# Performance work log

Measured on AMD Instinct MI355X. Metric: run time of the kernel, lower is better.

## Reference

```python
import jax, jax.numpy as jnp
import numpy as np

B, Z, A, D = 2048, 128, 4, 50000
EPS = 1e-8


def setup_inputs() -> dict:
    key = jax.random.key(0)
    k1, k2, k3, k4, k5 = jax.random.split(key, 5)
    return {
        "batch_x": jax.random.normal(k1, (B, Z), dtype=jnp.float32),
        "batch_next": jax.random.normal(k2, (B, Z), dtype=jnp.float32),
        "keys": jax.random.normal(k3, (A, D, Z), dtype=jnp.float32),
        "vals": jax.random.normal(k4, (A, D, Z), dtype=jnp.float32),
        "batch_a": jax.random.randint(k5, (B,), 0, A, dtype=jnp.int64),
    }


def _dnd_lookup(q, keys_a, vals_a):
    # q: [B, Z] (L2-normalized), keys_a: [D, Z], vals_a: [D, Z]
    kn = keys_a / (jnp.linalg.norm(keys_a, axis=-1, keepdims=True) + EPS)
    sims = jnp.einsum("bz,dz->bd", q, kn)          # cosine similarity [B, D]
    w = jax.nn.softmax(sims, axis=-1)                # attention over dictionary
    return jnp.einsum("bd,dz->bz", w, vals_a)       # [B, Z]


def reference(batch_x, batch_next, keys, vals, batch_a):
    # Per-sample routed DND lookup: each sample queries the memory of its action,
    # then MSE loss vs batch_next (eval-mode trainBatch; memory write is a state
    # mutation done after the loss and does not affect the returned value).
    qn = batch_x / (jnp.linalg.norm(batch_x, axis=-1, keepdims=True) + EPS)
    a_space = keys.shape[0]
    pred = jnp.zeros_like(batch_x)
    for a in range(a_space):  # small fixed loop over distinct memories
        pred_a = _dnd_lookup(qn, keys[a], vals[a])
        pred = jnp.where((batch_a == a)[:, None], pred_a, pred)
    return jnp.mean((pred - batch_next) ** 2)
```

## Files before the change

kernel.cpp:

```cpp
#include <hip/hip_runtime.h>
#include <stdint.h>

#define B_N 2048
#define Z_N 128
#define A_N 4
#define D_N 50000
#define EPS_F 1e-8f

typedef __attribute__((ext_vector_type(8))) short short8;
typedef __attribute__((ext_vector_type(4))) short bf4;
typedef __attribute__((ext_vector_type(4))) float f32x4;

__device__ __forceinline__ unsigned short f2bf(float f) {
  unsigned int u = __builtin_bit_cast(unsigned int, f);
  u += 0x7FFFu + ((u >> 16) & 1u);
  return (unsigned short)(u >> 16);
}

__global__ void k_norm(const float* __restrict__ keys, const float* __restrict__ x,
                       const int* __restrict__ act,
                       unsigned short* __restrict__ kn, unsigned short* __restrict__ qnb,
                       int* __restrict__ counts, int* __restrict__ lists) {
  int w = threadIdx.x >> 6, lane = threadIdx.x & 63;
  size_t row = (size_t)blockIdx.x * 4 + w;
  bool isq = row >= (size_t)A_N * D_N;
  size_t r = isq ? row - (size_t)A_N * D_N : row;
  const float* src = (isq ? x : keys) + r * Z_N;
  const float2 v = ((const float2*)src)[lane];
  float ss = v.x * v.x + v.y * v.y;
#pragma unroll
  for (int m = 1; m < 64; m <<= 1) ss += __shfl_xor(ss, m);
  float inv = 1.0f / (sqrtf(ss) + EPS_F);
  unsigned int packed = ((unsigned int)f2bf(v.y * inv) << 16) | f2bf(v.x * inv);
  unsigned short* dst = (isq ? qnb : kn) + r * Z_N;
  ((unsigned int*)dst)[lane] = packed;
  if (isq && lane == 0) {
    int a = act[r];
    int pos = atomicAdd(&counts[a], 1);
    lists[a * B_N + pos] = (int)r;
  }
}

__global__ void k_vtrans(const float* __restrict__ vals, unsigned short* __restrict__ vt) {
  __shared__ float tile[64][65];
  int a = blockIdx.z, d0 = blockIdx.x * 64, z0 = blockIdx.y * 64;
  int t = threadIdx.x;
  int r = t >> 4, c4 = (t & 15) * 4;
#pragma unroll
  for (int i = 0; i < 4; ++i) {
    int dr = r + i * 16, d = d0 + dr;
    if (d < D_N) {
      const float4 v = *(const float4*)(vals + ((size_t)a * D_N + d) * Z_N + z0 + c4);
      tile[dr][c4 + 0] = v.x; tile[dr][c4 + 1] = v.y;
      tile[dr][c4 + 2] = v.z; tile[dr][c4 + 3] = v.w;
    }
  }
  __syncthreads();
  int zz = t >> 2, dg = (t & 3) * 16;
  if (d0 + dg < D_N) {
    union { unsigned short u[16]; uint4 q[2]; } pk;
#pragma unroll
    for (int j = 0; j < 16; ++j) pk.u[j] = f2bf(tile[dg + j][zz]);
    unsigned short* dst = vt + ((size_t)a * Z_N + z0 + zz) * D_N + d0 + dg;
    ((uint4*)dst)[0] = pk.q[0];
    ((uint4*)dst)[1] = pk.q[1];
  }
}

#define TILE_B 128
#define KT 32
#define CHUNK 800
#define NITER 25
#define NCHUNK 63
#define KL_S 140
#define VL_S 36

__global__ void k_worklist(const int* __restrict__ counts, int* __restrict__ work) {
  int t0 = (counts[0] + TILE_B - 1) / TILE_B;
  int t1 = (counts[1] + TILE_B - 1) / TILE_B;
  int t2 = (counts[2] + TILE_B - 1) / TILE_B;
  int t3 = (counts[3] + TILE_B - 1) / TILE_B;
  int T = t0 + t1 + t2 + t3;
  int total = T * NCHUNK;
  if (threadIdx.x == 0) work[0] = total;
  for (int i = threadIdx.x; i < total; i += 256) {
    int c = i / T, j = i - c * T;
    int a, ty;
    if (j < t0)                { a = 0; ty = j; }
    else if (j < t0 + t1)      { a = 1; ty = j - t0; }
    else if (j < t0 + t1 + t2) { a = 2; ty = j - t0 - t1; }
    else                       { a = 3; ty = j - t0 - t1 - t2; }
    work[1 + i] = a | (ty << 2) | (c << 8);
  }
}

__launch_bounds__(256, 2)
__global__ void k_flash(const unsigned short* __restrict__ kn,
                        const unsigned short* __restrict__ vt,
                        const unsigned short* __restrict__ qnb,
                        const int* __restrict__ counts,
                        const int* __restrict__ lists,
                        const int* __restrict__ work,
                        float* __restrict__ acc,
                        float* __restrict__ sume) {
  int total = work[0];
  if ((int)blockIdx.x >= total) return;
  int wi = work[1 + blockIdx.x];
  int a = wi & 3, ty = (wi >> 2) & 63, chunk = wi >> 8;
  int nb = counts[a];

  __shared__ unsigned short Kl[KT * KL_S];
  __shared__ unsigned short Vl[128 * VL_S];

  int t = threadIdx.x;
  int w = t >> 6, lane = t & 63;
  int lq = lane >> 4, ln = lane & 15;

  const unsigned short* kn_a = kn + (size_t)a * D_N * Z_N;
  const unsigned short* vt_a = vt + (size_t)a * Z_N * D_N;
  const int* list_a = lists + a * B_N;

  short8 qf[2][4];
#pragma unroll
  for (int mt = 0; mt < 2; ++mt) {
    int g = ty * TILE_B + w * 32 + mt * 16 + ln;
    bool valid = g < nb;
    int si = valid ? list_a[g] : 0;
#pragma unroll
    for (int c = 0; c < 4; ++c) {
      short8 s = (short8){0,0,0,0,0,0,0,0};
      if (valid) s = *(const short8*)(qnb + (size_t)si * Z_N + c * 32 + lq * 8);
      qf[mt][c] = s;
    }
  }

  f32x4 O[2][8];
#pragma unroll
  for (int mt = 0; mt < 2; ++mt)
#pragma unroll
    for (int zt = 0; zt < 8; ++zt) O[mt][zt] = (f32x4){0.f, 0.f, 0.f, 0.f};
  float rs[2] = {0.f, 0.f};

  int d_base = chunk * CHUNK;
  int sk_key = t >> 3, sk_z = (t & 7) * 16;
  int sv_z = t >> 1, sv_k = (t & 1) * 16;

  const uint4 z4 = {0u, 0u, 0u, 0u};
  uint4 kA, kB, vA, vB;

  {
    int key = d_base + sk_key;
    bool kok = key < D_N;
    const uint4* ksrc = (const uint4*)(kn_a + (size_t)key * Z_N + sk_z);
    kA = kok ? ksrc[0] : z4;
    kB = kok ? ksrc[1] : z4;
    int kk = d_base + sv_k;
    const unsigned short* vsrc = vt_a + (size_t)sv_z * D_N + kk;
    vA = (kk < D_N)     ? *(const uint4*)vsrc       : z4;
    vB = (kk + 8 < D_N) ? *(const uint4*)(vsrc + 8) : z4;
  }

  for (int kt = 0; kt < NITER; ++kt) {
    int d0 = d_base + kt * KT;
    __syncthreads();
    {
      uint4* kd = (uint4*)&Kl[sk_key * KL_S + sk_z];
      kd[0] = kA; kd[1] = kB;
      uint4* vd = (uint4*)&Vl[sv_z * VL_S + sv_k];
      vd[0] = vA; vd[1] = vB;
    }
    __syncthreads();
    if (kt + 1 < NITER) {
      int d1 = d0 + KT;
      int key = d1 + sk_key;
      bool kok = key < D_N;
      const uint4* ksrc = (const uint4*)(kn_a + (size_t)key * Z_N + sk_z);
      kA = kok ? ksrc[0] : z4;
      kB = kok ? ksrc[1] : z4;
      int kk = d1 + sv_k;
      const unsigned short* vsrc = vt_a + (size_t)sv_z * D_N + kk;
      vA = (kk < D_N)     ? *(const uint4*)vsrc       : z4;
      vB = (kk + 8 < D_N) ? *(const uint4*)(vsrc + 8) : z4;
    }

    f32x4 ST[2][2];
#pragma unroll
    for (int nt = 0; nt < 2; ++nt) {
      short8 kf[4];
#pragma unroll
      for (int c = 0; c < 4; ++c)
        kf[c] = *(const short8*)&Kl[(nt * 16 + ln) * KL_S + c * 32 + lq * 8];
#pragma unroll
      for (int mt = 0; mt < 2; ++mt) {
        f32x4 s4 = (f32x4){0.f, 0.f, 0.f, 0.f};
#pragma unroll
        for (int c = 0; c < 4; ++c)
          s4 = __builtin_amdgcn_mfma_f32_16x16x32_bf16(kf[c], qf[mt][c], s4, 0, 0, 0);
        ST[nt][mt] = s4;
      }
    }

    bf4 pf[2][2];
#pragma unroll
    for (int nt = 0; nt < 2; ++nt) {
      int kbase = d0 + nt * 16 + lq * 4;
#pragma unroll
      for (int mt = 0; mt < 2; ++mt) {
        float e0 = (kbase + 0) < D_N ? __expf(ST[nt][mt][0]) : 0.f;
        float e1 = (kbase + 1) < D_N ? __expf(ST[nt][mt][1]) : 0.f;
        float e2 = (kbase + 2) < D_N ? __expf(ST[nt][mt][2]) : 0.f;
        float e3 = (kbase + 3) < D_N ? __expf(ST[nt][mt][3]) : 0.f;
        rs[mt] += e0 + e1 + e2 + e3;
        unsigned long long p =
            (unsigned long long)f2bf(e0) |
            ((unsigned long long)f2bf(e1) << 16) |
            ((unsigned long long)f2bf(e2) << 32) |
            ((unsigned long long)f2bf(e3) << 48);
        pf[mt][nt] = __builtin_bit_cast(bf4, p);
      }
    }

#pragma unroll
    for (int zt = 0; zt < 8; ++zt) {
#pragma unroll
      for (int nt = 0; nt < 2; ++nt) {
        bf4 vf = *(const bf4*)&Vl[(zt * 16 + ln) * VL_S + nt * 16 + lq * 4];
        asm volatile("s_nop 1\n\tv_mfma_f32_16x16x16_bf16 %0, %1, %2, %0"
                     : "+v"(O[0][zt]) : "v"(pf[0][nt]), "v"(vf));
        asm volatile("s_nop 1\n\tv_mfma_f32_16x16x16_bf16 %0, %1, %2, %0"
                     : "+v"(O[1][zt]) : "v"(pf[1][nt]), "v"(vf));
      }
    }
  }

#pragma unroll
  for (int mt = 0; mt < 2; ++mt) {
    float v = rs[mt];
    v += __shfl_xor(v, 16);
    v += __shfl_xor(v, 32);
    rs[mt] = v;
  }

#pragma unroll
  for (int mt = 0; mt < 2; ++mt) {
    if (lq == 0) {
      int g = ty * TILE_B + w * 32 + mt * 16 + ln;
      if (g < nb) atomicAdd(&sume[list_a[g]], rs[mt]);
    }
#pragma unroll
    for (int r = 0; r < 4; ++r) {
      int g = ty * TILE_B + w * 32 + mt * 16 + lq * 4 + r;
      if (g < nb) {
        int si = list_a[g];
        float* arow = acc + (size_t)si * Z_N + ln;
#pragma unroll
        for (int zt = 0; zt < 8; ++zt) atomicAdd(arow + zt * 16, O[mt][zt][r]);
      }
    }
  }
}

__global__ void k_loss(const float* __restrict__ acc, const float* __restrict__ sume,
                       const float* __restrict__ nxt, float* __restrict__ loss) {
  __shared__ float ls[4];
  int w = threadIdx.x >> 6, lane = threadIdx.x & 63;
  int row = blockIdx.x * 4 + w;
  float inv = 1.0f / sume[row];
  const float2 p2 = ((const float2*)(acc + (size_t)row * Z_N))[lane];
  const float2 n2 = ((const float2*)(nxt + (size_t)row * Z_N))[lane];
  float dx = p2.x * inv - n2.x, dy = p2.y * inv - n2.y;
  float s = dx * dx + dy * dy;
#pragma unroll
  for (int m = 1; m < 64; m <<= 1) s += __shfl_xor(s, m);
  if (lane == 0) ls[w] = s;
  __syncthreads();
  if (threadIdx.x == 0) atomicAdd(loss, ls[0] + ls[1] + ls[2] + ls[3]);
}

__global__ void k_final(const float* __restrict__ loss, float* __restrict__ out) {
  out[0] = loss[0] * (1.0f / (float)(B_N * Z_N));
}

extern "C" void kernel_launch(void* const* d_in, const int* in_sizes, int n_in,
                              void* d_out, int out_size, void* d_ws, size_t ws_size,
                              hipStream_t stream) {
  const float* x    = (const float*)d_in[0];
  const float* nxt  = (const float*)d_in[1];
  const float* keys = (const float*)d_in[2];
  const float* vals = (const float*)d_in[3];
  const int*   act  = (const int*)d_in[4];

  char* ws = (char*)d_ws;
  unsigned short* qnb = (unsigned short*)(ws + 0);
  float* acc    = (float*)(ws + 1048576);
  float* sume   = (float*)(ws + 2097152);
  int*   counts = (int*)(ws + 2105344);
  float* loss   = (float*)(ws + 2105360);
  int*   lists  = (int*)(ws + 2105376);
  int*   work   = (int*)(ws + 2138144);
  unsigned short* kn = (unsigned short*)(ws + 2146560);
  unsigned short* vt = (unsigned short*)(ws + 53346560);

  hipMemsetAsync(ws + 1048576, 0, 1056800, stream);

  k_norm<<<50512, 256, 0, stream>>>(keys, x, act, kn, qnb, counts, lists);
  k_vtrans<<<dim3(782, 2, A_N), 256, 0, stream>>>(vals, vt);
  k_worklist<<<1, 256, 0, stream>>>(counts, work);
  k_flash<<<1280, 256, 0, stream>>>(kn, vt, qnb, counts, lists, work, acc, sume);
  k_loss<<<512, 256, 0, stream>>>(acc, sume, nxt, loss);
  k_final<<<1, 1, 0, stream>>>(loss, (float*)d_out);
}
```

Before: 452.8 us.

## Restructure flash kernel to 512-thread blocks with double-buffered LDS and fewer splits

The flash-style lookup kernel now uses 512 threads per block, each wave owning 16 query rows instead of 32. Keys and transposed values are staged through double-buffered shared memory, so each iteration needs one barrier instead of two. The key dimension is split into 32 spans of 1568 rather than 63 chunks of 800, which roughly halves the number of partial-result atomics. Routing of samples by action moves out of the normalization kernel into a single-block kernel that counts in shared memory, removing global atomics on the counts. The trade-offs are less register reuse of each LDS fragment per wave and fewer blocks available to fill the GPU.

```diff
diff --git a/kernel.cpp b/kernel.cpp
--- a/kernel.cpp
+++ b/kernel.cpp
@@ -7,6 +7,14 @@
 #define D_N 50000
 #define EPS_F 1e-8f
 
+#define TILE_B 128
+#define KT 32
+#define NSPLIT 32
+#define SPAN 1568
+#define NITER 49
+#define KL_S 140
+#define VL_S 36
+
 typedef __attribute__((ext_vector_type(8))) short short8;
 typedef __attribute__((ext_vector_type(4))) short bf4;
 typedef __attribute__((ext_vector_type(4))) float f32x4;
@@ -18,9 +26,7 @@
 }
 
 __global__ void k_norm(const float* __restrict__ keys, const float* __restrict__ x,
-                       const int* __restrict__ act,
-                       unsigned short* __restrict__ kn, unsigned short* __restrict__ qnb,
-                       int* __restrict__ counts, int* __restrict__ lists) {
+                       unsigned short* __restrict__ kn, unsigned short* __restrict__ qnb) {
   int w = threadIdx.x >> 6, lane = threadIdx.x & 63;
   size_t row = (size_t)blockIdx.x * 4 + w;
   bool isq = row >= (size_t)A_N * D_N;
@@ -34,11 +40,6 @@
   unsigned int packed = ((unsigned int)f2bf(v.y * inv) << 16) | f2bf(v.x * inv);
   unsigned short* dst = (isq ? qnb : kn) + r * Z_N;
   ((unsigned int*)dst)[lane] = packed;
-  if (isq && lane == 0) {
-    int a = act[r];
-    int pos = atomicAdd(&counts[a], 1);
-    lists[a * B_N + pos] = (int)r;
-  }
 }
 
 __global__ void k_vtrans(const float* __restrict__ vals, unsigned short* __restrict__ vt) {
@@ -67,23 +68,25 @@
   }
 }
 
-#define TILE_B 128
-#define KT 32
-#define CHUNK 800
-#define NITER 25
-#define NCHUNK 63
-#define KL_S 140
-#define VL_S 36
-
-__global__ void k_worklist(const int* __restrict__ counts, int* __restrict__ work) {
-  int t0 = (counts[0] + TILE_B - 1) / TILE_B;
-  int t1 = (counts[1] + TILE_B - 1) / TILE_B;
-  int t2 = (counts[2] + TILE_B - 1) / TILE_B;
-  int t3 = (counts[3] + TILE_B - 1) / TILE_B;
+__global__ void k_route(const int* __restrict__ act, int* __restrict__ counts,
+                        int* __restrict__ lists, int* __restrict__ work) {
+  __shared__ int lc[4];
+  int t = threadIdx.x;
+  if (t < 4) lc[t] = 0;
+  __syncthreads();
+  for (int i = t; i < B_N; i += 1024) {
+    int a = act[i];
+    int pos = atomicAdd(&lc[a], 1);
+    lists[a * B_N + pos] = i;
+  }
+  __syncthreads();
+  if (t < 4) counts[t] = lc[t];
+  int t0 = (lc[0] + TILE_B - 1) >> 7, t1 = (lc[1] + TILE_B - 1) >> 7;
+  int t2 = (lc[2] + TILE_B - 1) >> 7, t3 = (lc[3] + TILE_B - 1) >> 7;
   int T = t0 + t1 + t2 + t3;
-  int total = T * NCHUNK;
-  if (threadIdx.x == 0) work[0] = total;
-  for (int i = threadIdx.x; i < total; i += 256) {
+  int total = T * NSPLIT;
+  if (t == 0) work[0] = total;
+  for (int i = t; i < total; i += 1024) {
     int c = i / T, j = i - c * T;
     int a, ty;
     if (j < t0)                { a = 0; ty = j; }
@@ -94,7 +97,7 @@
   }
 }
 
-__launch_bounds__(256, 2)
+__launch_bounds__(512)
 __global__ void k_flash(const unsigned short* __restrict__ kn,
                         const unsigned short* __restrict__ vt,
                         const unsigned short* __restrict__ qnb,
@@ -106,11 +109,11 @@
   int total = work[0];
   if ((int)blockIdx.x >= total) return;
   int wi = work[1 + blockIdx.x];
-  int a = wi & 3, ty = (wi >> 2) & 63, chunk = wi >> 8;
+  int a = wi & 3, ty = (wi >> 2) & 63, span = wi >> 8;
   int nb = counts[a];
 
-  __shared__ unsigned short Kl[KT * KL_S];
-  __shared__ unsigned short Vl[128 * VL_S];
+  __shared__ unsigned short Kl[2][KT * KL_S];
+  __shared__ unsigned short Vl[2][128 * VL_S];
 
   int t = threadIdx.x;
   int w = t >> 6, lane = t & 63;
@@ -120,142 +123,112 @@
   const unsigned short* vt_a = vt + (size_t)a * Z_N * D_N;
   const int* list_a = lists + a * B_N;
 
-  short8 qf[2][4];
-#pragma unroll
-  for (int mt = 0; mt < 2; ++mt) {
-    int g = ty * TILE_B + w * 32 + mt * 16 + ln;
-    bool valid = g < nb;
-    int si = valid ? list_a[g] : 0;
-#pragma unroll
-    for (int c = 0; c < 4; ++c) {
-      short8 s = (short8){0,0,0,0,0,0,0,0};
-      if (valid) s = *(const short8*)(qnb + (size_t)si * Z_N + c * 32 + lq * 8);
-      qf[mt][c] = s;
-    }
-  }
-
-  f32x4 O[2][8];
-#pragma unroll
-  for (int mt = 0; mt < 2; ++mt)
-#pragma unroll
-    for (int zt = 0; zt < 8; ++zt) O[mt][zt] = (f32x4){0.f, 0.f, 0.f, 0.f};
-  float rs[2] = {0.f, 0.f};
-
-  int d_base = chunk * CHUNK;
-  int sk_key = t >> 3, sk_z = (t & 7) * 16;
-  int sv_z = t >> 1, sv_k = (t & 1) * 16;
+  int g0 = ty * TILE_B + w * 16 + ln;
+  bool qvalid = g0 < nb;
+  int si0 = qvalid ? list_a[g0] : 0;
+  short8 qf[4];
+#pragma unroll
+  for (int c = 0; c < 4; ++c) {
+    short8 s = (short8){0,0,0,0,0,0,0,0};
+    if (qvalid) s = *(const short8*)(qnb + (size_t)si0 * Z_N + c * 32 + lq * 8);
+    qf[c] = s;
+  }
+
+  f32x4 O[8];
+#pragma unroll
+  for (int zt = 0; zt < 8; ++zt) O[zt] = (f32x4){0.f, 0.f, 0.f, 0.f};
+  float rs = 0.f;
+
+  int d_base = span * SPAN;
+  int sk_key = t >> 4, sk_z = (t & 15) * 8;
+  int sv_z = t >> 2, sv_k = (t & 3) * 8;
 
   const uint4 z4 = {0u, 0u, 0u, 0u};
-  uint4 kA, kB, vA, vB;
-
-  {
-    int key = d_base + sk_key;
-    bool kok = key < D_N;
-    const uint4* ksrc = (const uint4*)(kn_a + (size_t)key * Z_N + sk_z);
-    kA = kok ? ksrc[0] : z4;
-    kB = kok ? ksrc[1] : z4;
-    int kk = d_base + sv_k;
-    const unsigned short* vsrc = vt_a + (size_t)sv_z * D_N + kk;
-    vA = (kk < D_N)     ? *(const uint4*)vsrc       : z4;
-    vB = (kk + 8 < D_N) ? *(const uint4*)(vsrc + 8) : z4;
-  }
-
+  uint4 kp, vp;
+
+#define LOAD_TILE(d)                                                          \
+  {                                                                           \
+    int key = (d) + sk_key;                                                   \
+    kp = (key < D_N) ? *(const uint4*)(kn_a + (size_t)key * Z_N + sk_z) : z4; \
+    int kk = (d) + sv_k;                                                      \
+    vp = (kk < D_N) ? *(const uint4*)(vt_a + (size_t)sv_z * D_N + kk) : z4;   \
+  }
+#define STORE_TILE(p)                                                         \
+  {                                                                           \
+    *(uint4*)&Kl[p][sk_key * KL_S + sk_z] = kp;                               \
+    *(uint4*)&Vl[p][sv_z * VL_S + sv_k] = vp;                                 \
+  }
+
+  LOAD_TILE(d_base);
+  STORE_TILE(0);
+  LOAD_TILE(d_base + KT);
+  __syncthreads();
+
+  int p = 0;
   for (int kt = 0; kt < NITER; ++kt) {
     int d0 = d_base + kt * KT;
-    __syncthreads();
-    {
-      uint4* kd = (uint4*)&Kl[sk_key * KL_S + sk_z];
-      kd[0] = kA; kd[1] = kB;
-      uint4* vd = (uint4*)&Vl[sv_z * VL_S + sv_k];
-      vd[0] = vA; vd[1] = vB;
-    }
-    __syncthreads();
     if (kt + 1 < NITER) {
-      int d1 = d0 + KT;
-      int key = d1 + sk_key;
-      bool kok = key < D_N;
-      const uint4* ksrc = (const uint4*)(kn_a + (size_t)key * Z_N + sk_z);
-      kA = kok ? ksrc[0] : z4;
-      kB = kok ? ksrc[1] : z4;
-      int kk = d1 + sv_k;
-      const unsigned short* vsrc = vt_a + (size_t)sv_z * D_N + kk;
-      vA = (kk < D_N)     ? *(const uint4*)vsrc       : z4;
-      vB = (kk + 8 < D_N) ? *(const uint4*)(vsrc + 8) : z4;
-    }
-
-    f32x4 ST[2][2];
+      STORE_TILE(p ^ 1);
+      if (kt + 2 < NITER) LOAD_TILE(d0 + 2 * KT)
+    }
+
+    f32x4 ST[2];
 #pragma unroll
     for (int nt = 0; nt < 2; ++nt) {
       short8 kf[4];
 #pragma unroll
       for (int c = 0; c < 4; ++c)
-        kf[c] = *(const short8*)&Kl[(nt * 16 + ln) * KL_S + c * 32 + lq * 8];
-#pragma unroll
-      for (int mt = 0; mt < 2; ++mt) {
-        f32x4 s4 = (f32x4){0.f, 0.f, 0.f, 0.f};
-#pragma unroll
-        for (int c = 0; c < 4; ++c)
-          s4 = __builtin_amdgcn_mfma_f32_16x16x32_bf16(kf[c], qf[mt][c], s4, 0, 0, 0);
-        ST[nt][mt] = s4;
-      }
-    }
-
-    bf4 pf[2][2];
+        kf[c] = *(const short8*)&Kl[p][(nt * 16 + ln) * KL_S + c * 32 + lq * 8];
+      f32x4 s4 = (f32x4){0.f, 0.f, 0.f, 0.f};
+#pragma unroll
+      for (int c = 0; c < 4; ++c)
+        s4 = __builtin_amdgcn_mfma_f32_16x16x32_bf16(kf[c], qf[c], s4, 0, 0, 0);
+      ST[nt] = s4;
+    }
+
+    bf4 pf[2];
 #pragma unroll
     for (int nt = 0; nt < 2; ++nt) {
       int kbase = d0 + nt * 16 + lq * 4;
-#pragma unroll
-      for (int mt = 0; mt < 2; ++mt) {
-        float e0 = (kbase + 0) < D_N ? __expf(ST[nt][mt][0]) : 0.f;
-        float e1 = (kbase + 1) < D_N ? __expf(ST[nt][mt][1]) : 0.f;
-        float e2 = (kbase + 2) < D_N ? __expf(ST[nt][mt][2]) : 0.f;
-        float e3 = (kbase + 3) < D_N ? __expf(ST[nt][mt][3]) : 0.f;
-        rs[mt] += e0 + e1 + e2 + e3;
-        unsigned long long p =
-            (unsigned long long)f2bf(e0) |
-            ((unsigned long long)f2bf(e1) << 16) |
-            ((unsigned long long)f2bf(e2) << 32) |
-            ((unsigned long long)f2bf(e3) << 48);
-        pf[mt][nt] = __builtin_bit_cast(bf4, p);
+      float e0 = (kbase + 0) < D_N ? __expf(ST[nt][0]) : 0.f;
+      float e1 = (kbase + 1) < D_N ? __expf(ST[nt][1]) : 0.f;
+      float e2 = (kbase + 2) < D_N ? __expf(ST[nt][2]) : 0.f;
+      float e3 = (kbase + 3) < D_N ? __expf(ST[nt][3]) : 0.f;
+      rs += e0 + e1 + e2 + e3;
+      unsigned long long pk =
+          (unsigned long long)f2bf(e0) |
+          ((unsigned long long)f2bf(e1) << 16) |
+          ((unsigned long long)f2bf(e2) << 32) |
+          ((unsigned long long)f2bf(e3) << 48);
+      pf[nt] = __builtin_bit_cast(bf4, pk);
+    }
+
+#pragma unroll
+    for (int zt = 0; zt < 8; ++zt) {
+#pragma unroll
+      for (int nt = 0; nt < 2; ++nt) {
+        bf4 vf = *(const bf4*)&Vl[p][(zt * 16 + ln) * VL_S + nt * 16 + lq * 4];
+        asm volatile("s_nop 1\n\tv_mfma_f32_16x16x16_bf16 %0, %1, %2, %0"
+                     : "+v"(O[zt]) : "v"(pf[nt]), "v"(vf));
       }
     }
 
-#pragma unroll
-    for (int zt = 0; zt < 8; ++zt) {
-#pragma unroll
-      for (int nt = 0; nt < 2; ++nt) {
-        bf4 vf = *(const bf4*)&Vl[(zt * 16 + ln) * VL_S + nt * 16 + lq * 4];
-        asm volatile("s_nop 1\n\tv_mfma_f32_16x16x16_bf16 %0, %1, %2, %0"
-                     : "+v"(O[0][zt]) : "v"(pf[0][nt]), "v"(vf));
-        asm volatile("s_nop 1\n\tv_mfma_f32_16x16x16_bf16 %0, %1, %2, %0"
-                     : "+v"(O[1][zt]) : "v"(pf[1][nt]), "v"(vf));
-      }
-    }
-  }
-
-#pragma unroll
-  for (int mt = 0; mt < 2; ++mt) {
-    float v = rs[mt];
-    v += __shfl_xor(v, 16);
-    v += __shfl_xor(v, 32);
-    rs[mt] = v;
-  }
-
-#pragma unroll
-  for (int mt = 0; mt < 2; ++mt) {
-    if (lq == 0) {
-      int g = ty * TILE_B + w * 32 + mt * 16 + ln;
-      if (g < nb) atomicAdd(&sume[list_a[g]], rs[mt]);
-    }
-#pragma unroll
-    for (int r = 0; r < 4; ++r) {
-      int g = ty * TILE_B + w * 32 + mt * 16 + lq * 4 + r;
-      if (g < nb) {
-        int si = list_a[g];
-        float* arow = acc + (size_t)si * Z_N + ln;
-#pragma unroll
-        for (int zt = 0; zt < 8; ++zt) atomicAdd(arow + zt * 16, O[mt][zt][r]);
-      }
+    __syncthreads();
+    p ^= 1;
+  }
+
+  rs += __shfl_xor(rs, 16);
+  rs += __shfl_xor(rs, 32);
+
+  if (lq == 0 && qvalid) atomicAdd(&sume[si0], rs);
+#pragma unroll
+  for (int r = 0; r < 4; ++r) {
+    int g = ty * TILE_B + w * 16 + lq * 4 + r;
+    if (g < nb) {
+      int si = list_a[g];
+      float* arow = acc + (size_t)si * Z_N + ln;
+#pragma unroll
+      for (int zt = 0; zt < 8; ++zt) atomicAdd(arow + zt * 16, O[zt][r]);
     }
   }
 }
@@ -291,22 +264,22 @@
   const int*   act  = (const int*)d_in[4];
 
   char* ws = (char*)d_ws;
-  unsigned short* qnb = (unsigned short*)(ws + 0);
-  float* acc    = (float*)(ws + 1048576);
-  float* sume   = (float*)(ws + 2097152);
-  int*   counts = (int*)(ws + 2105344);
-  float* loss   = (float*)(ws + 2105360);
-  int*   lists  = (int*)(ws + 2105376);
-  int*   work   = (int*)(ws + 2138144);
-  unsigned short* kn = (unsigned short*)(ws + 2146560);
-  unsigned short* vt = (unsigned short*)(ws + 53346560);
-
-  hipMemsetAsync(ws + 1048576, 0, 1056800, stream);
-
-  k_norm<<<50512, 256, 0, stream>>>(keys, x, act, kn, qnb, counts, lists);
+  float* acc    = (float*)(ws + 0);
+  float* sume   = (float*)(ws + 1048576);
+  float* loss   = (float*)(ws + 1056768);
+  int*   counts = (int*)(ws + 1056784);
+  int*   lists  = (int*)(ws + 1056800);
+  int*   work   = (int*)(ws + 1089568);
+  unsigned short* qnb = (unsigned short*)(ws + 1093664);
+  unsigned short* kn  = (unsigned short*)(ws + 1617952);
+  unsigned short* vt  = (unsigned short*)(ws + 52817952);
+
+  hipMemsetAsync(ws, 0, 1056784, stream);
+
+  k_norm<<<50512, 256, 0, stream>>>(keys, x, kn, qnb);
   k_vtrans<<<dim3(782, 2, A_N), 256, 0, stream>>>(vals, vt);
-  k_worklist<<<1, 256, 0, stream>>>(counts, work);
-  k_flash<<<1280, 256, 0, stream>>>(kn, vt, qnb, counts, lists, work, acc, sume);
+  k_route<<<1, 1024, 0, stream>>>(act, counts, lists, work);
+  k_flash<<<640, 512, 0, stream>>>(kn, vt, qnb, counts, lists, work, acc, sume);
   k_loss<<<512, 256, 0, stream>>>(acc, sume, nxt, loss);
   k_final<<<1, 1, 0, stream>>>(loss, (float*)d_out);
 }
```

Result: faster. 421.5 us (-6.9%).
